# Kernel optimization log

Hardware: AMD Instinct MI355X
Metric: run time of the kernel (lower is better)

Reference implementation:

```python
import jax, jax.numpy as jnp
import numpy as np

# PointPillars PillarFeatureNet defaults
VX, VY, VZ = 0.2, 0.2, 4.0
X_OFF = VX / 2 + 0.0
Y_OFF = VY / 2 + (-40.0)
Z_OFF = VZ / 2 + (-3.0)
BN_EPS = 1e-3
N, M, C_RAW, C_IN, C_OUT = 100000, 32, 4, 10, 64


def setup_inputs() -> dict:
    key = jax.random.key(0)
    k1, k2, k3, k4, k5, k6 = jax.random.split(key, 6)
    features = jax.random.normal(k1, (N, M, C_RAW), dtype=jnp.float32)
    num_points = jax.random.randint(k2, (N,), 1, M + 1, dtype=jnp.int32)
    coors = jax.random.randint(k3, (N, 4), 0, 400, dtype=jnp.int32)
    # PFNLayer params: Linear(10 -> 64, bias=False) + BatchNorm1d(64) (eval stats)
    W = jax.random.normal(k4, (C_OUT, C_IN), dtype=jnp.float32) * (1.0 / np.sqrt(C_IN))
    gamma = jnp.ones((C_OUT,), jnp.float32)
    beta = jnp.zeros((C_OUT,), jnp.float32)
    running_mean = jax.random.normal(k5, (C_OUT,), dtype=jnp.float32) * 0.1
    running_var = jnp.abs(jax.random.normal(k6, (C_OUT,), dtype=jnp.float32)) * 0.1 + 0.9
    return {"features": features, "num_points": num_points, "coors": coors,
            "W": W, "gamma": gamma, "beta": beta,
            "running_mean": running_mean, "running_var": running_var}


def reference(features, num_points, coors, W, gamma, beta, running_mean, running_var):
    np_f = num_points.astype(features.dtype)[:, None, None]            # (N,1,1)
    xyz = features[:, :, :3]                                           # (N,M,3)
    # cluster center offset
    points_mean = jnp.sum(xyz, axis=1, keepdims=True) / np_f           # (N,1,3)
    f_cluster = xyz - points_mean                                      # (N,M,3)
    # voxel center offset (coors layout: [batch, z, y, x])
    cz = coors[:, 0].astype(features.dtype)[:, None]
    cy = coors[:, 1].astype(features.dtype)[:, None]
    cx = coors[:, 2].astype(features.dtype)[:, None]
    f_center = jnp.stack([
        features[:, :, 0] - (cx * VX + X_OFF),
        features[:, :, 1] - (cy * VY + Y_OFF),
        features[:, :, 2] - (cz * VZ + Z_OFF),
    ], axis=-1)                                                        # (N,M,3)
    feats = jnp.concatenate([features, f_cluster, f_center], axis=-1)  # (N,M,10)
    # padding mask
    mask = (jnp.arange(M, dtype=jnp.int32)[None, :] < num_points[:, None])
    feats = feats * mask[:, :, None].astype(feats.dtype)
    # PFNLayer: Linear -> BN(eval) -> GELU -> max over points
    x = jnp.einsum('nmc,oc->nmo', feats, W)                            # (N,M,64)
    inv_std = jax.lax.rsqrt(running_var + BN_EPS)
    x = (x - running_mean) * (inv_std * gamma) + beta
    x = jax.nn.gelu(x, approximate=False)
    return jnp.max(x, axis=1)                                          # (N,64)
```

## Files before the change

kernel.cpp:

```cpp
#include <hip/hip_runtime.h>
#include <cmath>


typedef float f32x2 __attribute__((ext_vector_type(2)));

__device__ __forceinline__ float max3f(float a, float b, float c) {
    float d;
    asm("v_max3_f32 %0, %1, %2, %3" : "=v"(d) : "v"(a), "v"(b), "v"(c));
    return d;
}
__device__ __forceinline__ float min3f(float a, float b, float c) {
    float d;
    asm("v_min3_f32 %0, %1, %2, %3" : "=v"(d) : "v"(a), "v"(b), "v"(c));
    return d;
}
__device__ __forceinline__ f32x2 pk_fma(f32x2 a, f32x2 b, f32x2 c) {
    f32x2 d;
    asm("v_pk_fma_f32 %0, %1, %2, %3" : "=v"(d) : "v"(a), "v"(b), "v"(c));
    return d;
}
__device__ __forceinline__ f32x2 pk_mul(f32x2 a, f32x2 b) {
    f32x2 d;
    asm("v_pk_mul_f32 %0, %1, %2" : "=v"(d) : "v"(a), "v"(b));
    return d;
}
__device__ __forceinline__ float fast_exp2(float a) {
    float d;
    asm("v_exp_f32 %0, %1" : "=v"(d) : "v"(a));
    return d;
}

__device__ __forceinline__ f32x2 gelu2(f32x2 x) {
    const f32x2 c_t    = {0.70710678f, 0.70710678f};
    const f32x2 c_p    = {0.3275911f, 0.3275911f};
    const f32x2 c_one  = {1.0f, 1.0f};
    const f32x2 b1 = {-0.254829592f, -0.254829592f};
    const f32x2 b2 = { 0.284496736f,  0.284496736f};
    const f32x2 b3 = {-1.421413741f, -1.421413741f};
    const f32x2 b4 = { 1.453152027f,  1.453152027f};
    const f32x2 b5 = {-1.061405429f, -1.061405429f};
    const f32x2 c_k = {-1.02013963f, -1.02013963f};

    f32x2 ax = {fabsf(x.x), fabsf(x.y)};
    f32x2 t  = pk_mul(ax, c_t);
    f32x2 u  = pk_fma(t, c_p, c_one);
    f32x2 s  = {__builtin_amdgcn_rcpf(u.x), __builtin_amdgcn_rcpf(u.y)};
    f32x2 poly = pk_fma(b5, s, b4);
    poly = pk_fma(poly, s, b3);
    poly = pk_fma(poly, s, b2);
    poly = pk_fma(poly, s, b1);
    poly = pk_mul(poly, s);
    f32x2 t3  = pk_mul(ax, c_k);
    f32x2 arg = pk_mul(t, t3);
    f32x2 e   = {fast_exp2(arg.x), fast_exp2(arg.y)};
    f32x2 E   = pk_fma(poly, e, c_one);
    f32x2 h   = pk_mul(x, (f32x2){0.5f, 0.5f});
    f32x2 hax = pk_mul(ax, (f32x2){0.5f, 0.5f});
    return pk_fma(hax, E, h);
}

template <int CTRL, int ROW_MASK>
__device__ __forceinline__ float dpp_add(float v) {
    int x = __builtin_amdgcn_update_dpp(0, __builtin_bit_cast(int, v), CTRL, ROW_MASK, 0xf, false);
    return v + __builtin_bit_cast(float, x);
}
__device__ __forceinline__ void half_sums(float v, float& sA, float& sB) {
    v = dpp_add<0x111, 0xf>(v);
    v = dpp_add<0x112, 0xf>(v);
    v = dpp_add<0x114, 0xf>(v);
    v = dpp_add<0x118, 0xf>(v);
    v = dpp_add<0x142, 0xa>(v);
    sA = __builtin_bit_cast(float, __builtin_amdgcn_readlane(__builtin_bit_cast(int, v), 31));
    sB = __builtin_bit_cast(float, __builtin_amdgcn_readlane(__builtin_bit_cast(int, v), 63));
}

__device__ __forceinline__ float bcast0_half(float v) {
    int x = __builtin_amdgcn_ds_swizzle(__builtin_bit_cast(int, v), 0x0000);
    return __builtin_bit_cast(float, x);
}

__device__ __forceinline__ void scan16(const float4* base,
                                       float A0, float A1, float A2, float A3,
                                       float& mx0, float& mn0, float& mx1, float& mn1) {
    #pragma unroll
    for (int m = 0; m < 16; m += 4) {
        float4 t0 = base[m], t1 = base[m + 1], t2 = base[m + 2], t3 = base[m + 3];
        float y0 = fmaf(t0.x, A0, fmaf(t0.y, A1, fmaf(t0.z, A2, t0.w * A3)));
        float y1 = fmaf(t1.x, A0, fmaf(t1.y, A1, fmaf(t1.z, A2, t1.w * A3)));
        float y2 = fmaf(t2.x, A0, fmaf(t2.y, A1, fmaf(t2.z, A2, t2.w * A3)));
        float y3 = fmaf(t3.x, A0, fmaf(t3.y, A1, fmaf(t3.z, A2, t3.w * A3)));
        mx0 = max3f(mx0, y0, y1); mn0 = min3f(mn0, y0, y1);
        mx1 = max3f(mx1, y2, y3); mn1 = min3f(mn1, y2, y3);
    }
}
__device__ __forceinline__ void scan_pillar(const float4* base, int n,
                                            float A0, float A1, float A2, float A3,
                                            float& dmax, float& dmin) {
    float mx0 = -INFINITY, mn0 = INFINITY, mx1 = -INFINITY, mn1 = INFINITY;
    scan16(base, A0, A1, A2, A3, mx0, mn0, mx1, mn1);
    if (n > 16)
        scan16(base + 16, A0, A1, A2, A3, mx0, mn0, mx1, mn1);
    dmax = fmaxf(mx0, mx1);
    dmin = fminf(mn0, mn1);
}

__global__ __launch_bounds__(256) void pfn_kernel(
    const float* __restrict__ features,
    const int*   __restrict__ num_points,
    const int*   __restrict__ coors,
    const float* __restrict__ W,
    const float* __restrict__ gamma,
    const float* __restrict__ beta,
    const float* __restrict__ rmean,
    const float* __restrict__ rvar,
    float*       __restrict__ out,
    int nTotal)
{
    __shared__ float4 lds[512];

    const int lane = threadIdx.x & 63;
    const int wid  = threadIdx.x >> 6;
    const int wv   = blockIdx.x * 4 + wid;
    const int nPairs = (nTotal + 1) >> 1;
    const int p0 = wv * 2;
    if (p0 >= nPairs) return;
    const int p1 = (p0 + 1 < nPairs) ? (p0 + 1) : p0;

    const float4* fbase = reinterpret_cast<const float4*>(features);
    const float4 f0 = fbase[(size_t)p0 * 64 + lane];
    const float4 f1 = fbase[(size_t)p1 * 64 + lane];

    const int i0A = 2 * p0;
    const bool h0B = (2 * p0 + 1 < nTotal);
    const int i0B = h0B ? (2 * p0 + 1) : (nTotal - 1);
    const int i1A = 2 * p1;
    const bool h1B = (2 * p1 + 1 < nTotal);
    const int i1B = h1B ? (2 * p1 + 1) : (nTotal - 1);

    const int n0A = num_points[i0A], n0B = num_points[i0B];
    const int n1A = num_points[i1A], n1B = num_points[i1B];
    const int4 c0A = reinterpret_cast<const int4*>(coors)[i0A];
    const int4 c0B = reinterpret_cast<const int4*>(coors)[i0B];
    const int4 c1A = reinterpret_cast<const int4*>(coors)[i1A];
    const int4 c1B = reinterpret_cast<const int4*>(coors)[i1B];

    const int o = lane;
    const float w4 = W[o*10+4], w5 = W[o*10+5], w6 = W[o*10+6], w7 = W[o*10+7],
                w8 = W[o*10+8], w9 = W[o*10+9];
    const float w0 = W[o*10+0], w1 = W[o*10+1], w2 = W[o*10+2], w3 = W[o*10+3];
    const float a = gamma[o] / sqrtf(rvar[o] + 1e-3f);
    const float b = fmaf(-rmean[o], a, beta[o]);
    const float A0 = a*(w0+w4+w7), A1 = a*(w1+w5+w8), A2 = a*(w2+w6+w9), A3 = a*w3;

    float4 q0, q1;
    q0.x = bcast0_half(f0.x); q0.y = bcast0_half(f0.y);
    q0.z = bcast0_half(f0.z); q0.w = bcast0_half(f0.w);
    q1.x = bcast0_half(f1.x); q1.y = bcast0_half(f1.y);
    q1.z = bcast0_half(f1.z); q1.w = bcast0_half(f1.w);

    const int pt = lane & 31;
    const int vn0 = (lane < 32) ? n0A : n0B;
    const int vn1 = (lane < 32) ? n1A : n1B;
    const float4 st0 = (pt < vn0) ? f0 : q0;
    const float4 st1 = (pt < vn1) ? f1 : q1;

    float4* slot = &lds[wid * 128];
    slot[lane]      = st0;
    slot[64 + lane] = st1;

    float s0Ax, s0Bx, s0Ay, s0By, s0Az, s0Bz;
    float s1Ax, s1Bx, s1Ay, s1By, s1Az, s1Bz;
    half_sums(f0.x, s0Ax, s0Bx);
    half_sums(f0.y, s0Ay, s0By);
    half_sums(f0.z, s0Az, s0Bz);
    half_sums(f1.x, s1Ax, s1Bx);
    half_sums(f1.y, s1Ay, s1By);
    half_sums(f1.z, s1Az, s1Bz);

    const float rc0A = __builtin_amdgcn_rcpf((float)n0A);
    const float rc0B = __builtin_amdgcn_rcpf((float)n0B);
    const float rc1A = __builtin_amdgcn_rcpf((float)n1A);
    const float rc1B = __builtin_amdgcn_rcpf((float)n1B);

    const float K0A = -((s0Ax*rc0A)*w4 + (s0Ay*rc0A)*w5 + (s0Az*rc0A)*w6
                      + fmaf((float)c0A.z, 0.2f, 0.1f)*w7
                      + fmaf((float)c0A.y, 0.2f, -39.9f)*w8
                      + fmaf((float)c0A.x, 4.0f, -1.0f)*w9);
    const float K0B = -((s0Bx*rc0B)*w4 + (s0By*rc0B)*w5 + (s0Bz*rc0B)*w6
                      + fmaf((float)c0B.z, 0.2f, 0.1f)*w7
                      + fmaf((float)c0B.y, 0.2f, -39.9f)*w8
                      + fmaf((float)c0B.x, 4.0f, -1.0f)*w9);
    const float K1A = -((s1Ax*rc1A)*w4 + (s1Ay*rc1A)*w5 + (s1Az*rc1A)*w6
                      + fmaf((float)c1A.z, 0.2f, 0.1f)*w7
                      + fmaf((float)c1A.y, 0.2f, -39.9f)*w8
                      + fmaf((float)c1A.x, 4.0f, -1.0f)*w9);
    const float K1B = -((s1Bx*rc1B)*w4 + (s1By*rc1B)*w5 + (s1Bz*rc1B)*w6
                      + fmaf((float)c1B.z, 0.2f, 0.1f)*w7
                      + fmaf((float)c1B.y, 0.2f, -39.9f)*w8
                      + fmaf((float)c1B.x, 4.0f, -1.0f)*w9);
    const float C0A = fmaf(a, K0A, b), C0B = fmaf(a, K0B, b);
    const float C1A = fmaf(a, K1A, b), C1B = fmaf(a, K1B, b);

    asm volatile("" ::: "memory");

    float d0Amax, d0Amin, d0Bmax, d0Bmin, d1Amax, d1Amin, d1Bmax, d1Bmin;
    scan_pillar(slot,      n0A, A0, A1, A2, A3, d0Amax, d0Amin);
    scan_pillar(slot + 32, n0B, A0, A1, A2, A3, d0Bmax, d0Bmin);
    scan_pillar(slot + 64, n1A, A0, A1, A2, A3, d1Amax, d1Amin);
    scan_pillar(slot + 96, n1B, A0, A1, A2, A3, d1Bmax, d1Bmin);

    float vmax0A = d0Amax + C0A, vmin0A = d0Amin + C0A;
    float vmax0B = d0Bmax + C0B, vmin0B = d0Bmin + C0B;
    float vmax1A = d1Amax + C1A, vmin1A = d1Amin + C1A;
    float vmax1B = d1Bmax + C1B, vmin1B = d1Bmin + C1B;

    if (n0A < 32) { vmax0A = fmaxf(vmax0A, b); vmin0A = fminf(vmin0A, b); }
    if (n0B < 32) { vmax0B = fmaxf(vmax0B, b); vmin0B = fminf(vmin0B, b); }
    if (n1A < 32) { vmax1A = fmaxf(vmax1A, b); vmin1A = fminf(vmin1A, b); }
    if (n1B < 32) { vmax1B = fmaxf(vmax1B, b); vmin1B = fminf(vmin1B, b); }

    const f32x2 g0A = gelu2((f32x2){vmax0A, vmin0A});
    const f32x2 g0B = gelu2((f32x2){vmax0B, vmin0B});
    const f32x2 g1A = gelu2((f32x2){vmax1A, vmin1A});
    const f32x2 g1B = gelu2((f32x2){vmax1B, vmin1B});

    out[(size_t)i0A * 64 + o] = fmaxf(g0A.x, g0A.y);
    if (h0B) out[(size_t)i0B * 64 + o] = fmaxf(g0B.x, g0B.y);
    out[(size_t)i1A * 64 + o] = fmaxf(g1A.x, g1A.y);
    if (h1B) out[(size_t)i1B * 64 + o] = fmaxf(g1B.x, g1B.y);
}

extern "C" void kernel_launch(void* const* d_in, const int* in_sizes, int n_in,
                              void* d_out, int out_size, void* d_ws, size_t ws_size,
                              hipStream_t stream) {
    const float* features   = (const float*)d_in[0];
    const int*   num_points = (const int*)  d_in[1];
    const int*   coors      = (const int*)  d_in[2];
    const float* W          = (const float*)d_in[3];
    const float* gamma      = (const float*)d_in[4];
    const float* beta       = (const float*)d_in[5];
    const float* rmean      = (const float*)d_in[6];
    const float* rvar       = (const float*)d_in[7];
    float* out = (float*)d_out;

    const int nTotal = in_sizes[1];

    const int nPairs = (nTotal + 1) / 2;
    int blocks = (nPairs + 7) / 8;
    if (blocks < 1) blocks = 1;
    pfn_kernel<<<blocks, 256, 0, stream>>>(features, num_points, coors, W,
                                           gamma, beta, rmean, rvar, out, nTotal);
}
```

Measured before the change: 123.7 us.

## Use persistent grid-stride waves with next-pillar prefetch and exact-length point scan

The kernel becomes persistent: a capped grid of waves loops over pillar pairs and loads the next iteration's features, num_points and coors before processing the current ones, so global-load latency overlaps compute. The scan now walks only the valid points, in chunks of 8 plus a remainder loop. This lets the masked-lane broadcast (ds_swizzle) and padded LDS stores be dropped. Risks are extra register pressure from the prefetched values, and more divergent branching in the remainder loop.

```diff
diff --git a/kernel.cpp b/kernel.cpp
--- a/kernel.cpp
+++ b/kernel.cpp
@@ -74,32 +74,47 @@
     sB = __builtin_bit_cast(float, __builtin_amdgcn_readlane(__builtin_bit_cast(int, v), 63));
 }
 
-__device__ __forceinline__ float bcast0_half(float v) {
-    int x = __builtin_amdgcn_ds_swizzle(__builtin_bit_cast(int, v), 0x0000);
-    return __builtin_bit_cast(float, x);
-}
-
-__device__ __forceinline__ void scan16(const float4* base,
-                                       float A0, float A1, float A2, float A3,
-                                       float& mx0, float& mn0, float& mx1, float& mn1) {
-    #pragma unroll
-    for (int m = 0; m < 16; m += 4) {
-        float4 t0 = base[m], t1 = base[m + 1], t2 = base[m + 2], t3 = base[m + 3];
-        float y0 = fmaf(t0.x, A0, fmaf(t0.y, A1, fmaf(t0.z, A2, t0.w * A3)));
-        float y1 = fmaf(t1.x, A0, fmaf(t1.y, A1, fmaf(t1.z, A2, t1.w * A3)));
-        float y2 = fmaf(t2.x, A0, fmaf(t2.y, A1, fmaf(t2.z, A2, t2.w * A3)));
-        float y3 = fmaf(t3.x, A0, fmaf(t3.y, A1, fmaf(t3.z, A2, t3.w * A3)));
-        mx0 = max3f(mx0, y0, y1); mn0 = min3f(mn0, y0, y1);
-        mx1 = max3f(mx1, y2, y3); mn1 = min3f(mn1, y2, y3);
-    }
-}
+__device__ __forceinline__ void scan8(const float4* b4,
+                                      float A0, float A1, float A2, float A3,
+                                      float& mx0, float& mn0, float& mx1, float& mn1) {
+    float4 t0 = b4[0], t1 = b4[1], t2 = b4[2], t3 = b4[3];
+    float4 t4 = b4[4], t5 = b4[5], t6 = b4[6], t7 = b4[7];
+    float y0 = fmaf(t0.x, A0, fmaf(t0.y, A1, fmaf(t0.z, A2, t0.w * A3)));
+    float y1 = fmaf(t1.x, A0, fmaf(t1.y, A1, fmaf(t1.z, A2, t1.w * A3)));
+    float y2 = fmaf(t2.x, A0, fmaf(t2.y, A1, fmaf(t2.z, A2, t2.w * A3)));
+    float y3 = fmaf(t3.x, A0, fmaf(t3.y, A1, fmaf(t3.z, A2, t3.w * A3)));
+    float y4 = fmaf(t4.x, A0, fmaf(t4.y, A1, fmaf(t4.z, A2, t4.w * A3)));
+    float y5 = fmaf(t5.x, A0, fmaf(t5.y, A1, fmaf(t5.z, A2, t5.w * A3)));
+    float y6 = fmaf(t6.x, A0, fmaf(t6.y, A1, fmaf(t6.z, A2, t6.w * A3)));
+    float y7 = fmaf(t7.x, A0, fmaf(t7.y, A1, fmaf(t7.z, A2, t7.w * A3)));
+    mx0 = max3f(mx0, y0, y1); mn0 = min3f(mn0, y0, y1);
+    mx1 = max3f(mx1, y2, y3); mn1 = min3f(mn1, y2, y3);
+    mx0 = max3f(mx0, y4, y5); mn0 = min3f(mn0, y4, y5);
+    mx1 = max3f(mx1, y6, y7); mn1 = min3f(mn1, y6, y7);
+}
+
 __device__ __forceinline__ void scan_pillar(const float4* base, int n,
                                             float A0, float A1, float A2, float A3,
                                             float& dmax, float& dmin) {
     float mx0 = -INFINITY, mn0 = INFINITY, mx1 = -INFINITY, mn1 = INFINITY;
-    scan16(base, A0, A1, A2, A3, mx0, mn0, mx1, mn1);
-    if (n > 16)
-        scan16(base + 16, A0, A1, A2, A3, mx0, mn0, mx1, mn1);
+    const int nfull = n >> 3;
+    if (nfull > 0) scan8(base,      A0, A1, A2, A3, mx0, mn0, mx1, mn1);
+    if (nfull > 1) scan8(base + 8,  A0, A1, A2, A3, mx0, mn0, mx1, mn1);
+    if (nfull > 2) scan8(base + 16, A0, A1, A2, A3, mx0, mn0, mx1, mn1);
+    if (nfull > 3) scan8(base + 24, A0, A1, A2, A3, mx0, mn0, mx1, mn1);
+    const int rem = n & 7;
+    if (rem) {
+        const float4* br = base + (nfull << 3);
+        #pragma unroll
+        for (int j = 0; j < 7; ++j) {
+            if (j < rem) {
+                float4 t = br[j];
+                float y = fmaf(t.x, A0, fmaf(t.y, A1, fmaf(t.z, A2, t.w * A3)));
+                mx0 = fmaxf(mx0, y);
+                mn0 = fminf(mn0, y);
+            }
+        }
+    }
     dmax = fmaxf(mx0, mx1);
     dmin = fminf(mn0, mn1);
 }
@@ -121,113 +136,133 @@
     const int lane = threadIdx.x & 63;
     const int wid  = threadIdx.x >> 6;
     const int wv   = blockIdx.x * 4 + wid;
-    const int nPairs = (nTotal + 1) >> 1;
-    const int p0 = wv * 2;
-    if (p0 >= nPairs) return;
-    const int p1 = (p0 + 1 < nPairs) ? (p0 + 1) : p0;
-
-    const float4* fbase = reinterpret_cast<const float4*>(features);
-    const float4 f0 = fbase[(size_t)p0 * 64 + lane];
-    const float4 f1 = fbase[(size_t)p1 * 64 + lane];
-
-    const int i0A = 2 * p0;
-    const bool h0B = (2 * p0 + 1 < nTotal);
-    const int i0B = h0B ? (2 * p0 + 1) : (nTotal - 1);
-    const int i1A = 2 * p1;
-    const bool h1B = (2 * p1 + 1 < nTotal);
-    const int i1B = h1B ? (2 * p1 + 1) : (nTotal - 1);
-
-    const int n0A = num_points[i0A], n0B = num_points[i0B];
-    const int n1A = num_points[i1A], n1B = num_points[i1B];
-    const int4 c0A = reinterpret_cast<const int4*>(coors)[i0A];
-    const int4 c0B = reinterpret_cast<const int4*>(coors)[i0B];
-    const int4 c1A = reinterpret_cast<const int4*>(coors)[i1A];
-    const int4 c1B = reinterpret_cast<const int4*>(coors)[i1B];
+    const int nPairs  = (nTotal + 1) >> 1;
+    const int strideP = gridDim.x * 4 * 2;
+
+    int p = wv * 2;
+    if (p >= nPairs) return;
 
     const int o = lane;
-    const float w4 = W[o*10+4], w5 = W[o*10+5], w6 = W[o*10+6], w7 = W[o*10+7],
+    const float w0 = W[o*10+0], w1 = W[o*10+1], w2 = W[o*10+2], w3 = W[o*10+3],
+                w4 = W[o*10+4], w5 = W[o*10+5], w6 = W[o*10+6], w7 = W[o*10+7],
                 w8 = W[o*10+8], w9 = W[o*10+9];
-    const float w0 = W[o*10+0], w1 = W[o*10+1], w2 = W[o*10+2], w3 = W[o*10+3];
     const float a = gamma[o] / sqrtf(rvar[o] + 1e-3f);
     const float b = fmaf(-rmean[o], a, beta[o]);
     const float A0 = a*(w0+w4+w7), A1 = a*(w1+w5+w8), A2 = a*(w2+w6+w9), A3 = a*w3;
 
-    float4 q0, q1;
-    q0.x = bcast0_half(f0.x); q0.y = bcast0_half(f0.y);
-    q0.z = bcast0_half(f0.z); q0.w = bcast0_half(f0.w);
-    q1.x = bcast0_half(f1.x); q1.y = bcast0_half(f1.y);
-    q1.z = bcast0_half(f1.z); q1.w = bcast0_half(f1.w);
-
-    const int pt = lane & 31;
-    const int vn0 = (lane < 32) ? n0A : n0B;
-    const int vn1 = (lane < 32) ? n1A : n1B;
-    const float4 st0 = (pt < vn0) ? f0 : q0;
-    const float4 st1 = (pt < vn1) ? f1 : q1;
-
+    const float4* fbase = reinterpret_cast<const float4*>(features);
     float4* slot = &lds[wid * 128];
-    slot[lane]      = st0;
-    slot[64 + lane] = st1;
-
-    float s0Ax, s0Bx, s0Ay, s0By, s0Az, s0Bz;
-    float s1Ax, s1Bx, s1Ay, s1By, s1Az, s1Bz;
-    half_sums(f0.x, s0Ax, s0Bx);
-    half_sums(f0.y, s0Ay, s0By);
-    half_sums(f0.z, s0Az, s0Bz);
-    half_sums(f1.x, s1Ax, s1Bx);
-    half_sums(f1.y, s1Ay, s1By);
-    half_sums(f1.z, s1Az, s1Bz);
-
-    const float rc0A = __builtin_amdgcn_rcpf((float)n0A);
-    const float rc0B = __builtin_amdgcn_rcpf((float)n0B);
-    const float rc1A = __builtin_amdgcn_rcpf((float)n1A);
-    const float rc1B = __builtin_amdgcn_rcpf((float)n1B);
-
-    const float K0A = -((s0Ax*rc0A)*w4 + (s0Ay*rc0A)*w5 + (s0Az*rc0A)*w6
-                      + fmaf((float)c0A.z, 0.2f, 0.1f)*w7
-                      + fmaf((float)c0A.y, 0.2f, -39.9f)*w8
-                      + fmaf((float)c0A.x, 4.0f, -1.0f)*w9);
-    const float K0B = -((s0Bx*rc0B)*w4 + (s0By*rc0B)*w5 + (s0Bz*rc0B)*w6
-                      + fmaf((float)c0B.z, 0.2f, 0.1f)*w7
-                      + fmaf((float)c0B.y, 0.2f, -39.9f)*w8
-                      + fmaf((float)c0B.x, 4.0f, -1.0f)*w9);
-    const float K1A = -((s1Ax*rc1A)*w4 + (s1Ay*rc1A)*w5 + (s1Az*rc1A)*w6
-                      + fmaf((float)c1A.z, 0.2f, 0.1f)*w7
-                      + fmaf((float)c1A.y, 0.2f, -39.9f)*w8
-                      + fmaf((float)c1A.x, 4.0f, -1.0f)*w9);
-    const float K1B = -((s1Bx*rc1B)*w4 + (s1By*rc1B)*w5 + (s1Bz*rc1B)*w6
-                      + fmaf((float)c1B.z, 0.2f, 0.1f)*w7
-                      + fmaf((float)c1B.y, 0.2f, -39.9f)*w8
-                      + fmaf((float)c1B.x, 4.0f, -1.0f)*w9);
-    const float C0A = fmaf(a, K0A, b), C0B = fmaf(a, K0B, b);
-    const float C1A = fmaf(a, K1A, b), C1B = fmaf(a, K1B, b);
-
-    asm volatile("" ::: "memory");
-
-    float d0Amax, d0Amin, d0Bmax, d0Bmin, d1Amax, d1Amin, d1Bmax, d1Bmin;
-    scan_pillar(slot,      n0A, A0, A1, A2, A3, d0Amax, d0Amin);
-    scan_pillar(slot + 32, n0B, A0, A1, A2, A3, d0Bmax, d0Bmin);
-    scan_pillar(slot + 64, n1A, A0, A1, A2, A3, d1Amax, d1Amin);
-    scan_pillar(slot + 96, n1B, A0, A1, A2, A3, d1Bmax, d1Bmin);
-
-    float vmax0A = d0Amax + C0A, vmin0A = d0Amin + C0A;
-    float vmax0B = d0Bmax + C0B, vmin0B = d0Bmin + C0B;
-    float vmax1A = d1Amax + C1A, vmin1A = d1Amin + C1A;
-    float vmax1B = d1Bmax + C1B, vmin1B = d1Bmin + C1B;
-
-    if (n0A < 32) { vmax0A = fmaxf(vmax0A, b); vmin0A = fminf(vmin0A, b); }
-    if (n0B < 32) { vmax0B = fmaxf(vmax0B, b); vmin0B = fminf(vmin0B, b); }
-    if (n1A < 32) { vmax1A = fmaxf(vmax1A, b); vmin1A = fminf(vmin1A, b); }
-    if (n1B < 32) { vmax1B = fmaxf(vmax1B, b); vmin1B = fminf(vmin1B, b); }
-
-    const f32x2 g0A = gelu2((f32x2){vmax0A, vmin0A});
-    const f32x2 g0B = gelu2((f32x2){vmax0B, vmin0B});
-    const f32x2 g1A = gelu2((f32x2){vmax1A, vmin1A});
-    const f32x2 g1B = gelu2((f32x2){vmax1B, vmin1B});
-
-    out[(size_t)i0A * 64 + o] = fmaxf(g0A.x, g0A.y);
-    if (h0B) out[(size_t)i0B * 64 + o] = fmaxf(g0B.x, g0B.y);
-    out[(size_t)i1A * 64 + o] = fmaxf(g1A.x, g1A.y);
-    if (h1B) out[(size_t)i1B * 64 + o] = fmaxf(g1B.x, g1B.y);
+
+    int p1 = (p + 1 < nPairs) ? (p + 1) : p;
+    float4 f0 = fbase[(size_t)p * 64 + lane];
+    float4 f1 = fbase[(size_t)p1 * 64 + lane];
+    int iA0 = 2*p;
+    int iB0 = (2*p + 1 < nTotal) ? (2*p + 1) : (nTotal - 1);
+    int iA1 = 2*p1;
+    int iB1 = (2*p1 + 1 < nTotal) ? (2*p1 + 1) : (nTotal - 1);
+    int n0A = num_points[iA0], n0B = num_points[iB0];
+    int n1A = num_points[iA1], n1B = num_points[iB1];
+    int4 c0A = reinterpret_cast<const int4*>(coors)[iA0];
+    int4 c0B = reinterpret_cast<const int4*>(coors)[iB0];
+    int4 c1A = reinterpret_cast<const int4*>(coors)[iA1];
+    int4 c1B = reinterpret_cast<const int4*>(coors)[iB1];
+
+    for (;;) {
+        const int pn = p + strideP;
+        const bool hasNext = pn < nPairs;
+        float4 g0, g1;
+        int m0A = 0, m0B = 0, m1A = 0, m1B = 0;
+        int4 d0A, d0B, d1A, d1B;
+        int jA0 = 0, jB0 = 0, jA1 = 0, jB1 = 0;
+        if (hasNext) {
+            const int pn1 = (pn + 1 < nPairs) ? (pn + 1) : pn;
+            g0 = fbase[(size_t)pn * 64 + lane];
+            g1 = fbase[(size_t)pn1 * 64 + lane];
+            jA0 = 2*pn;
+            jB0 = (2*pn + 1 < nTotal) ? (2*pn + 1) : (nTotal - 1);
+            jA1 = 2*pn1;
+            jB1 = (2*pn1 + 1 < nTotal) ? (2*pn1 + 1) : (nTotal - 1);
+            m0A = num_points[jA0]; m0B = num_points[jB0];
+            m1A = num_points[jA1]; m1B = num_points[jB1];
+            d0A = reinterpret_cast<const int4*>(coors)[jA0];
+            d0B = reinterpret_cast<const int4*>(coors)[jB0];
+            d1A = reinterpret_cast<const int4*>(coors)[jA1];
+            d1B = reinterpret_cast<const int4*>(coors)[jB1];
+        }
+
+        slot[lane]      = f0;
+        slot[64 + lane] = f1;
+
+        float s0Ax, s0Bx, s0Ay, s0By, s0Az, s0Bz;
+        float s1Ax, s1Bx, s1Ay, s1By, s1Az, s1Bz;
+        half_sums(f0.x, s0Ax, s0Bx);
+        half_sums(f0.y, s0Ay, s0By);
+        half_sums(f0.z, s0Az, s0Bz);
+        half_sums(f1.x, s1Ax, s1Bx);
+        half_sums(f1.y, s1Ay, s1By);
+        half_sums(f1.z, s1Az, s1Bz);
+
+        const float rc0A = __builtin_amdgcn_rcpf((float)n0A);
+        const float rc0B = __builtin_amdgcn_rcpf((float)n0B);
+        const float rc1A = __builtin_amdgcn_rcpf((float)n1A);
+        const float rc1B = __builtin_amdgcn_rcpf((float)n1B);
+
+        const float K0A = -((s0Ax*rc0A)*w4 + (s0Ay*rc0A)*w5 + (s0Az*rc0A)*w6
+                          + fmaf((float)c0A.z, 0.2f, 0.1f)*w7
+                          + fmaf((float)c0A.y, 0.2f, -39.9f)*w8
+                          + fmaf((float)c0A.x, 4.0f, -1.0f)*w9);
+        const float K0B = -((s0Bx*rc0B)*w4 + (s0By*rc0B)*w5 + (s0Bz*rc0B)*w6
+                          + fmaf((float)c0B.z, 0.2f, 0.1f)*w7
+                          + fmaf((float)c0B.y, 0.2f, -39.9f)*w8
+                          + fmaf((float)c0B.x, 4.0f, -1.0f)*w9);
+        const float K1A = -((s1Ax*rc1A)*w4 + (s1Ay*rc1A)*w5 + (s1Az*rc1A)*w6
+                          + fmaf((float)c1A.z, 0.2f, 0.1f)*w7
+                          + fmaf((float)c1A.y, 0.2f, -39.9f)*w8
+                          + fmaf((float)c1A.x, 4.0f, -1.0f)*w9);
+        const float K1B = -((s1Bx*rc1B)*w4 + (s1By*rc1B)*w5 + (s1Bz*rc1B)*w6
+                          + fmaf((float)c1B.z, 0.2f, 0.1f)*w7
+                          + fmaf((float)c1B.y, 0.2f, -39.9f)*w8
+                          + fmaf((float)c1B.x, 4.0f, -1.0f)*w9);
+        const float C0A = fmaf(a, K0A, b), C0B = fmaf(a, K0B, b);
+        const float C1A = fmaf(a, K1A, b), C1B = fmaf(a, K1B, b);
+
+        asm volatile("" ::: "memory");
+
+        float d0Amax, d0Amin, d0Bmax, d0Bmin, d1Amax, d1Amin, d1Bmax, d1Bmin;
+        scan_pillar(slot,      n0A, A0, A1, A2, A3, d0Amax, d0Amin);
+        scan_pillar(slot + 32, n0B, A0, A1, A2, A3, d0Bmax, d0Bmin);
+        scan_pillar(slot + 64, n1A, A0, A1, A2, A3, d1Amax, d1Amin);
+        scan_pillar(slot + 96, n1B, A0, A1, A2, A3, d1Bmax, d1Bmin);
+
+        float vmax0A = d0Amax + C0A, vmin0A = d0Amin + C0A;
+        float vmax0B = d0Bmax + C0B, vmin0B = d0Bmin + C0B;
+        float vmax1A = d1Amax + C1A, vmin1A = d1Amin + C1A;
+        float vmax1B = d1Bmax + C1B, vmin1B = d1Bmin + C1B;
+
+        if (n0A < 32) { vmax0A = fmaxf(vmax0A, b); vmin0A = fminf(vmin0A, b); }
+        if (n0B < 32) { vmax0B = fmaxf(vmax0B, b); vmin0B = fminf(vmin0B, b); }
+        if (n1A < 32) { vmax1A = fmaxf(vmax1A, b); vmin1A = fminf(vmin1A, b); }
+        if (n1B < 32) { vmax1B = fmaxf(vmax1B, b); vmin1B = fminf(vmin1B, b); }
+
+        const f32x2 g0Ae = gelu2((f32x2){vmax0A, vmin0A});
+        const f32x2 g0Be = gelu2((f32x2){vmax0B, vmin0B});
+        const f32x2 g1Ae = gelu2((f32x2){vmax1A, vmin1A});
+        const f32x2 g1Be = gelu2((f32x2){vmax1B, vmin1B});
+
+        out[(size_t)iA0 * 64 + o] = fmaxf(g0Ae.x, g0Ae.y);
+        if (2*p + 1 < nTotal)  out[(size_t)iB0 * 64 + o] = fmaxf(g0Be.x, g0Be.y);
+        out[(size_t)iA1 * 64 + o] = fmaxf(g1Ae.x, g1Ae.y);
+        if (2*p1 + 1 < nTotal) out[(size_t)iB1 * 64 + o] = fmaxf(g1Be.x, g1Be.y);
+
+        if (!hasNext) break;
+
+        p  = pn;
+        p1 = (pn + 1 < nPairs) ? (pn + 1) : pn;
+        f0 = g0; f1 = g1;
+        iA0 = jA0; iB0 = jB0; iA1 = jA1; iB1 = jB1;
+        n0A = m0A; n0B = m0B; n1A = m1A; n1B = m1B;
+        c0A = d0A; c0B = d0B; c1A = d1A; c1B = d1B;
+    }
 }
 
 extern "C" void kernel_launch(void* const* d_in, const int* in_sizes, int n_in,
@@ -246,7 +281,9 @@
     const int nTotal = in_sizes[1];
 
     const int nPairs = (nTotal + 1) / 2;
-    int blocks = (nPairs + 7) / 8;
+    int blocks = 4096;
+    const int maxBlocks = (nPairs + 7) / 8;
+    if (blocks > maxBlocks) blocks = maxBlocks;
     if (blocks < 1) blocks = 1;
     pfn_kernel<<<blocks, 256, 0, stream>>>(features, num_points, coors, W,
                                            gamma, beta, rmean, rvar, out, nTotal);
```

New measurement: 131.1 us. +6.0%, slower.
